# Performance work log

Hardware: AMD Instinct MI355X
Metric: run time of the kernel (lower is better)

The kernel has to match this reference:

```python
import jax, jax.numpy as jnp
import numpy as np

IN_F = 135; D = 512; K = 10; DCT_N = 34; IN_N = 120; OUT_N = 24
VL = K + OUT_N          # 34, window length
VN = IN_N - K - OUT_N + 1  # 87, number of windows
NSTAGE = 2
BN_SCALE = 1.0 / np.sqrt(1.0 + 1e-5)  # eval-mode BN with default running stats (mean 0, var 1)


def get_dct_matrix(N):
    dct_m = np.eye(N)
    for k in range(N):
        for i in range(N):
            w = np.sqrt(2.0 / N)
            if k == 0:
                w = np.sqrt(1.0 / N)
            dct_m[k, i] = w * np.cos(np.pi * (i + 0.5) * k / N)
    idct_m = np.linalg.inv(dct_m)
    return dct_m, idct_m

_DCT_NP, _IDCT_NP = get_dct_matrix(VL)
DCT = jnp.asarray(_DCT_NP[:DCT_N], dtype=jnp.float32)        # [34,34] (dct_n == vl)
IDCT = jnp.asarray(_IDCT_NP[:, :DCT_N], dtype=jnp.float32)   # [34,34]

WIN_IDX = np.arange(VL)[None, :] + np.arange(VN)[:, None]    # [87,34]
PAD_IDX = np.concatenate([np.arange(IN_N - K, IN_N), np.full(OUT_N, IN_N - 1)])  # last 10 frames + last frame repeated


def conv1d(x, w):
    return jax.lax.conv_general_dilated(x, w, (1,), 'VALID',
                                        dimension_numbers=('NCH', 'OIH', 'NCH'))


def gconv(x, att, w, b):
    # GraphConvolution: att @ (x @ w) + b ; x: [b,n,f_in]
    return jnp.einsum('nm,bmf->bnf', att, x @ w) + b


def bn_eval(y, g, b):
    bs, n, f = y.shape
    v = y.reshape(bs, n * f)
    v = g * (v * BN_SCALE) + b
    return v.reshape(bs, n, f)


def setup_inputs() -> dict:
    key = jax.random.key(0)
    ks = jax.random.split(key, 20)
    s = 0.05  # small init scale so tanh/att stay in sane range
    return {
        'poses':    jax.random.normal(ks[0], (256, 144, 135), jnp.float32),
        'qw1':      jax.random.normal(ks[1], (512, 135, 6)) * s,
        'qw2':      jax.random.normal(ks[2], (512, 512, 5)) * s,
        'kw1':      jax.random.normal(ks[3], (512, 135, 6)) * s,
        'kw2':      jax.random.normal(ks[4], (512, 512, 5)) * s,
        'gc1_att':  jax.random.normal(ks[5], (135, 135)) * s,
        'gc1_w':    jax.random.normal(ks[6], (68, 512)) * s,
        'gc1_b':    jax.random.normal(ks[7], (512,)) * s,
        'bn1_g':    jnp.ones((69120,), jnp.float32),
        'bn1_b':    jnp.zeros((69120,), jnp.float32),
        'gcb_att':  jax.random.normal(ks[8], (4, 135, 135)) * s,
        'gcb_w':    jax.random.normal(ks[9], (4, 512, 512)) * s,
        'gcb_b':    jax.random.normal(ks[10], (4, 512)) * s,
        'gcb_g':    jnp.ones((4, 69120), jnp.float32),
        'gcb_beta': jnp.zeros((4, 69120), jnp.float32),
        'gc7_att':  jax.random.normal(ks[11], (135, 135)) * s,
        'gc7_w':    jax.random.normal(ks[12], (512, 68)) * s,
        'gc7_b':    jax.random.normal(ks[13], (68,)) * s,
    }


def reference(poses, qw1, qw2, kw1, kw2,
              gc1_att, gc1_w, gc1_b, bn1_g, bn1_b,
              gcb_att, gcb_w, gcb_b, gcb_g, gcb_beta,
              gc7_att, gc7_w, gc7_b):
    src = poses[:, :IN_N]                      # [b,120,135]
    bs = src.shape[0]
    src_t = jnp.transpose(src, (0, 2, 1))      # [b,135,120]
    key_in = src_t[:, :, :IN_N - OUT_N] / 1000.0   # [b,135,96]
    qry_in = src_t[:, :, -K:] / 1000.0             # [b,135,10]

    key_f = jax.nn.relu(conv1d(jax.nn.relu(conv1d(key_in, kw1)), kw2))  # [b,512,87]
    qry_f = jax.nn.relu(conv1d(jax.nn.relu(conv1d(qry_in, qw1)), qw2))  # [b,512,1]

    # non-softmax attention: matmul + eps-normalize
    score = jnp.einsum('bdq,bdk->bqk', qry_f, key_f) + 1e-15   # [b,1,87]
    att = score / jnp.sum(score, axis=2, keepdims=True)

    # overlapping windows -> DCT of each window
    windows = src[:, WIN_IDX]                                   # [b,87,34,135]
    val = jnp.einsum('kt,bvtf->bvfk', DCT, windows).reshape(bs, VN, IN_F * DCT_N)
    dct_att = jnp.einsum('bqv,bvz->bqz', att, val)[:, 0].reshape(bs, IN_F, DCT_N)

    input_gcn = src[:, PAD_IDX]                                 # [b,34,135]
    dct_in = jnp.einsum('kt,btf->bfk', DCT, input_gcn)          # [b,135,34]
    x = jnp.concatenate([dct_in, dct_att], axis=-1)             # [b,135,68]

    # GCN (eval mode: dropout = identity, BN uses running stats)
    y = jnp.tanh(bn_eval(gconv(x, gc1_att, gc1_w, gc1_b), bn1_g, bn1_b))
    for i in range(NSTAGE):
        res = y
        h = jnp.tanh(bn_eval(gconv(y, gcb_att[2 * i], gcb_w[2 * i], gcb_b[2 * i]),
                             gcb_g[2 * i], gcb_beta[2 * i]))
        h = jnp.tanh(bn_eval(gconv(h, gcb_att[2 * i + 1], gcb_w[2 * i + 1], gcb_b[2 * i + 1]),
                             gcb_g[2 * i + 1], gcb_beta[2 * i + 1]))
        y = h + res
    y = gconv(y, gc7_att, gc7_w, gc7_b) + x                     # [b,135,68]

    out = jnp.einsum('tk,bfk->btf', IDCT, y[:, :, :DCT_N])      # [b,34,135]
    preds = out[:, -OUT_N:, :]                                  # [b,24,135]
    return preds
```

## Files before the change

kernel.cpp:

```cpp
#include <hip/hip_runtime.h>
#include <math.h>

#define POSE_ROWS 144
#define NF 135
#define DD 512
#define KQ 10
#define DCTN 34
#define INN 120
#define OUTN 24
#define VN 87
#define BATCH 256
#define RP 34816
#define NODEP 136
#define BSTRIDE 69632
#define BN_SCALE 0.9999950000374997f

typedef __attribute__((ext_vector_type(8))) short short8;
typedef __attribute__((ext_vector_type(4))) float floatx4;

static __device__ __forceinline__ ushort f2bf(float f) {
    unsigned u = __builtin_bit_cast(unsigned, f);
    u = (u + 0x7FFFu + ((u >> 16) & 1u)) >> 16;
    return (ushort)u;
}
static __device__ __forceinline__ float bf2f(ushort s) {
    return __builtin_bit_cast(float, (unsigned)s << 16);
}
static __device__ __forceinline__ float tanh_fast(float x) {
    float ax = __builtin_fabsf(x);
    float e = __builtin_amdgcn_exp2f(ax * -2.885390081777927f);
    float t = (1.f - e) * __builtin_amdgcn_rcpf(1.f + e);
    return __builtin_copysignf(t, x);
}

#define GLOAD_LDS(gp, lp) __builtin_amdgcn_global_load_lds( \
    (const __attribute__((address_space(1))) unsigned int*)(const void*)(gp), \
    (__attribute__((address_space(3))) unsigned int*)(void*)(lp), 16, 0, 0)

#define PB_POSES 19584
#define PB_K1B   22912
#define PB_K2B   33152
#define PB_WT1   33408
#define PB_WTB   37504
#define PB_WT7   37640
#define PB_A1    37742
#define PB_AB    38147
#define PB_A7    38249
#define PB_BN    39609
#define PB_Z     39610
#define PB_DCT   39615

__global__ __launch_bounds__(256) void prep_all(
    const float* __restrict__ poses, ushort* __restrict__ pb16,
    const float* __restrict__ kw1, const float* __restrict__ qw1,
    ushort* __restrict__ Wt1k, ushort* __restrict__ Wt1q,
    const float* __restrict__ kw2, const float* __restrict__ qw2,
    ushort* __restrict__ Wt2k, ushort* __restrict__ Wt2q,
    const float* __restrict__ gc1_w, ushort* __restrict__ WT1,
    const float* __restrict__ gcb_w, ushort* __restrict__ WTb,
    const float* __restrict__ gc7_w, ushort* __restrict__ WT7,
    const float* __restrict__ gc1_att, ushort* __restrict__ A16_1,
    const float* __restrict__ gcb_att, ushort* __restrict__ A16_B,
    const float* __restrict__ gc7_att, ushort* __restrict__ A16_7,
    const float* __restrict__ bn1_g, const float* __restrict__ bn1_b,
    const float* __restrict__ gcb_g, const float* __restrict__ gcb_beta,
    float* __restrict__ bnT, float* __restrict__ zpadf, float* __restrict__ dct)
{
    const int blk = blockIdx.x;
    const int tid = threadIdx.x;
    if (blk < PB_POSES) {
        int idx = blk * 256 + tid;
        int i = idx % NODEP;
        int row = (idx / NODEP) % POSE_ROWS;
        int b = idx / (NODEP * POSE_ROWS);
        float v = (i < NF) ? poses[((long long)b * POSE_ROWS + row) * NF + i] * 1e-3f : 0.f;
        pb16[idx] = f2bf(v);
    } else if (blk < PB_K1B) {
        int wi = blk - PB_POSES;
        const float* src = (wi < 1664) ? kw1 : qw1;
        ushort* dst = (wi < 1664) ? Wt1k : Wt1q;
        int idx = (wi % 1664) * 256 + tid;
        int n = idx / 832, k = idx % 832;
        int h = k / 136, i = k % 136;
        float v = (i < 135 && h < 6) ? src[((long long)n * 135 + i) * 6 + h] : 0.f;
        dst[idx] = f2bf(v);
    } else if (blk < PB_K2B) {
        int wi = blk - PB_K1B;
        const float* src = (wi < 5120) ? kw2 : qw2;
        ushort* dst = (wi < 5120) ? Wt2k : Wt2q;
        int idx = (wi % 5120) * 256 + tid;
        int n = idx / 2560, k = idx % 2560;
        int h = k / 512, i = k % 512;
        dst[idx] = f2bf(src[((long long)n * 512 + i) * 5 + h]);
    } else if (blk < PB_WT1) {
        int idx = (blk - PB_K2B) * 256 + tid;
        int n = idx / 128, k = idx % 128;
        WT1[idx] = f2bf((k < 68) ? gc1_w[(long long)k * 512 + n] : 0.f);
    } else if (blk < PB_WTB) {
        int g = (blk - PB_WT1) * 256 + tid;
        int L = g >> 18, idx = g & 262143;
        int n = idx / 512, k = idx % 512;
        WTb[g] = f2bf(gcb_w[(long long)L * 262144 + (long long)k * 512 + n]);
    } else if (blk < PB_WT7) {
        int idx = (blk - PB_WTB) * 256 + tid;
        int n = idx / 512, k = idx % 512;
        WT7[idx] = f2bf(gc7_w[(long long)k * 68 + n]);
    } else if (blk < PB_A1) {
        int idx = (blk - PB_WT7) * 256 + tid;
        if (idx < 135 * 192) {
            int r = idx / 192, c = idx % 192;
            A16_1[idx] = f2bf(c < 135 ? gc1_att[r * 135 + c] : 0.f);
        }
    } else if (blk < PB_AB) {
        int idx = (blk - PB_A1) * 256 + tid;
        int r = idx / 192, c = idx % 192;
        A16_B[idx] = f2bf(c < 135 ? gcb_att[r * 135 + c] : 0.f);
    } else if (blk < PB_A7) {
        int idx = (blk - PB_AB) * 256 + tid;
        if (idx < 135 * 192) {
            int r = idx / 192, c = idx % 192;
            A16_7[idx] = f2bf(c < 135 ? gc7_att[r * 135 + c] : 0.f);
        }
    } else if (blk < PB_BN) {
        int g = (blk - PB_A7) * 256 + tid;
        int p = g / 69632, idx = g % 69632;
        int node = idx % 136, m = idx / 136;
        const float* gs = (p == 0) ? bn1_g : (gcb_g + (p - 1) * 69120);
        const float* bs = (p == 0) ? bn1_b : (gcb_beta + (p - 1) * 69120);
        float* gt = bnT + (long long)p * 139264;
        float* bt = gt + 69632;
        gt[idx] = (node < 135) ? gs[node * 512 + m] : 0.f;
        bt[idx] = (node < 135) ? bs[node * 512 + m] : 0.f;
    } else if (blk < PB_Z) {
        if (tid < 128) zpadf[tid] = 0.f;
    } else {
        int idx = (blk - PB_Z) * 256 + tid;
        if (idx < DCTN * DCTN) {
            int k = idx / DCTN, i = idx % DCTN;
            double w = (k == 0) ? sqrt(1.0 / DCTN) : sqrt(2.0 / DCTN);
            dct[idx] = (float)(w * cos(3.14159265358979323846 * (i + 0.5) * k / (double)DCTN));
        }
    }
}

template<int BM, int BN>
__global__ __launch_bounds__(256) void gemm2(
    const ushort* __restrict__ A, const ushort* __restrict__ Bt,
    const ushort* __restrict__ zpad,
    int M, int N, int K,
    int mode, int CNT, int Pc,
    int rpbA, long long sAw, long long sAr, long long sAbz,
    long long sBr, long long sBbz,
    float* __restrict__ C, ushort* __restrict__ C16,
    long long sCbz, long long sCm, long long sCn,
    int do_relu, const float* __restrict__ bias, int bias_mode,
    const float* __restrict__ bnTg, const float* __restrict__ bnTb,
    int do_tanh, const ushort* __restrict__ resid16, const float* __restrict__ resid32,
    int bmaj)
{
    constexpr int SM = BM / 32, SN = BN / 32;
    constexpr int RA = BM / 32, RB = BN / 32;
    __shared__ ushort As[BM * 64];
    __shared__ ushort Bs[BN * 64];

    int mb, nb;
    if (mode == 0) { mb = blockIdx.y; nb = blockIdx.x; }
    else {
        int gx = blockIdx.x;
        int x = gx & 7, s = gx >> 3;
        if (mode == 1) { mb = s % CNT; nb = x * Pc + s / CNT; }
        else           { nb = s % CNT; mb = x * Pc + s / CNT; }
    }
    const int m0 = mb * BM, n0 = nb * BN;
    if (m0 >= M || n0 >= N) return;

    const int tid = threadIdx.x;
    const int lane = tid & 63, w = tid >> 6;
    const int bz = blockIdx.z;
    const int wm = (w >> 1) * (BM / 2), wn = (w & 1) * (BN / 2);
    const int chunk = (lane & 7) ^ ((lane >> 3) & 7);

    const ushort* pA[RA]; int stA[RA];
    #pragma unroll
    for (int j = 0; j < RA; j++) {
        int m = m0 + j * 32 + w * 8 + (lane >> 3);
        bool v = m < M;
        long long off = v ? ((long long)(m / rpbA) * sAw + (long long)(m % rpbA) * sAr
                            + (long long)bz * sAbz) : 0;
        pA[j] = v ? (A + off + chunk * 8) : (zpad + chunk * 8);
        stA[j] = v ? 64 : 0;
    }
    const ushort* pB[RB]; int stB[RB];
    #pragma unroll
    for (int j = 0; j < RB; j++) {
        int n = n0 + j * 32 + w * 8 + (lane >> 3);
        bool v = n < N;
        long long off = v ? ((long long)n * sBr + (long long)bz * sBbz) : 0;
        pB[j] = v ? (Bt + off + chunk * 8) : (zpad + chunk * 8);
        stB[j] = v ? 64 : 0;
    }

    floatx4 acc[SM][SN];
    #pragma unroll
    for (int i = 0; i < SM; i++)
        #pragma unroll
        for (int j = 0; j < SN; j++)
            acc[i][j] = (floatx4){0.f, 0.f, 0.f, 0.f};

    for (int k0 = 0; k0 < K; k0 += 64) {
        #pragma unroll
        for (int j = 0; j < RA; j++)
            GLOAD_LDS(pA[j], &As[(j * 32 + w * 8) * 64]);
        #pragma unroll
        for (int j = 0; j < RB; j++)
            GLOAD_LDS(pB[j], &Bs[(j * 32 + w * 8) * 64]);
        __syncthreads();

        #pragma unroll
        for (int kk = 0; kk < 2; kk++) {
            short8 af[SM], bf[SN];
            #pragma unroll
            for (int sm = 0; sm < SM; sm++) {
                int lr = wm + sm * 16 + (lane & 15);
                int slot = ((lane >> 4) + kk * 4) ^ (lr & 7);
                af[sm] = *(const short8*)&As[lr * 64 + slot * 8];
            }
            #pragma unroll
            for (int sn = 0; sn < SN; sn++) {
                int lr = wn + sn * 16 + (lane & 15);
                int slot = ((lane >> 4) + kk * 4) ^ (lr & 7);
                bf[sn] = *(const short8*)&Bs[lr * 64 + slot * 8];
            }
            #pragma unroll
            for (int sm = 0; sm < SM; sm++)
                #pragma unroll
                for (int sn = 0; sn < SN; sn++)
                    acc[sm][sn] = __builtin_amdgcn_mfma_f32_16x16x32_bf16(af[sm], bf[sn], acc[sm][sn], 0, 0, 0);
        }
        __syncthreads();

        #pragma unroll
        for (int j = 0; j < RA; j++) pA[j] += stA[j];
        #pragma unroll
        for (int j = 0; j < RB; j++) pB[j] += stB[j];
    }

    const int lc = lane & 15;
    const int lr4 = (lane >> 4) << 2;
    #pragma unroll
    for (int sm = 0; sm < SM; sm++) {
        #pragma unroll
        for (int sn = 0; sn < SN; sn++) {
            int n = n0 + wn + sn * 16 + lc;
            if (n >= N) continue;
            int node = n % 136;
            int mbv = m0 + wm + sm * 16 + lr4;
            float vv[4];
            #pragma unroll
            for (int r = 0; r < 4; r++) {
                int m = mbv + r;
                float v = acc[sm][sn][r];
                if (do_relu) v = fmaxf(v, 0.f);
                if (bias) v += (bias_mode == 1) ? bias[m < M ? m : 0] : bias[n];
                if (bnTg) {
                    long long gi = (long long)(m < M ? m : 0) * 136 + node;
                    v = bnTg[gi] * (v * BN_SCALE) + bnTb[gi];
                }
                if (do_tanh) v = tanh_fast(v);
                long long addr = bmaj
                    ? (long long)(n / 136) * BSTRIDE + (long long)m * 136 + node
                    : (long long)bz * sCbz + (long long)m * sCm + (long long)n * sCn;
                if (m < M) {
                    if (resid16) v += bf2f(resid16[addr]);
                    else if (resid32) v += resid32[addr];
                    if (C) C[addr] = v;
                    if (C16 && sCm != 1) C16[addr] = f2bf(v);
                }
                vv[r] = v;
            }
            if (C16 && sCm == 1 && mbv + 3 < M) {
                ushort4 pk;
                pk.x = f2bf(vv[0]); pk.y = f2bf(vv[1]); pk.z = f2bf(vv[2]); pk.w = f2bf(vv[3]);
                *(ushort4*)&C16[(long long)bz * sCbz + mbv + (long long)n * sCn] = pk;
            }
        }
    }
}

__global__ __launch_bounds__(512) void fused_layer(
    const ushort* __restrict__ Yin,
    const ushort* __restrict__ Att,
    const ushort* __restrict__ Wt,
    const ushort* __restrict__ zpad,
    const float* __restrict__ bias,
    const float* __restrict__ bnTg, const float* __restrict__ bnTb,
    const ushort* __restrict__ resid16,
    ushort* __restrict__ Yout)
{
    extern __shared__ ushort zs[];
    const int b = blockIdx.x;
    const int tid = threadIdx.x;
    const int lane = tid & 63, w = tid >> 6;
    const int ln = lane & 15;
    const int lk8 = (lane >> 4) * 8;
    const int lr4 = (lane >> 4) << 2;
    const long long ybase = (long long)b * BSTRIDE;
    const int cp = w * 64;

    {
        const ushort* pb[9];
        #pragma unroll
        for (int nt = 0; nt < 9; nt++) {
            int n = nt * 16 + ln;
            pb[nt] = (n < 135) ? (Att + (long long)n * 192 + lk8) : (zpad + lk8);
        }
        const ushort* pa[4];
        #pragma unroll
        for (int sm = 0; sm < 4; sm++) {
            int c = cp + sm * 16 + ln;
            pa[sm] = Yin + ybase + (long long)c * 136 + lk8;
        }
        floatx4 acc[4][9];
        #pragma unroll
        for (int i = 0; i < 4; i++)
            #pragma unroll
            for (int j = 0; j < 9; j++)
                acc[i][j] = (floatx4){0.f, 0.f, 0.f, 0.f};

        #pragma unroll
        for (int ks = 0; ks < 5; ks++) {
            const int ko = ks * 32;
            short8 af[4];
            #pragma unroll
            for (int sm = 0; sm < 4; sm++)
                af[sm] = *(const short8*)(pa[sm] + ko);
            #pragma unroll
            for (int nt = 0; nt < 9; nt++) {
                short8 bfv = *(const short8*)(pb[nt] + ko);
                #pragma unroll
                for (int sm = 0; sm < 4; sm++)
                    acc[sm][nt] = __builtin_amdgcn_mfma_f32_16x16x32_bf16(af[sm], bfv, acc[sm][nt], 0, 0, 0);
            }
        }
        #pragma unroll
        for (int sm = 0; sm < 4; sm++) {
            #pragma unroll
            for (int nt = 0; nt < 9; nt++) {
                int n = nt * 16 + ln;
                if (n >= 136) continue;
                int c = cp + sm * 16 + lr4;
                ushort4 pk;
                pk.x = f2bf(acc[sm][nt][0]);
                pk.y = f2bf(acc[sm][nt][1]);
                pk.z = f2bf(acc[sm][nt][2]);
                pk.w = f2bf(acc[sm][nt][3]);
                int chs = (c >> 3) ^ (n & 7);
                *(ushort4*)&zs[n * 512 + chs * 8 + (c & 7)] = pk;
            }
        }
    }
    __syncthreads();

    {
        const ushort* pw[4];
        #pragma unroll
        for (int sm = 0; sm < 4; sm++)
            pw[sm] = Wt + (long long)(cp + sm * 16 + ln) * 512 + lk8;
        int zrow[9], zx[9];
        #pragma unroll
        for (int nt = 0; nt < 9; nt++) {
            int n = nt * 16 + ln;
            int nn = (n < 136) ? n : 0;
            zrow[nt] = nn * 512;
            zx[nt] = nn & 7;
        }
        floatx4 acc[4][9];
        #pragma unroll
        for (int i = 0; i < 4; i++)
            #pragma unroll
            for (int j = 0; j < 9; j++)
                acc[i][j] = (floatx4){0.f, 0.f, 0.f, 0.f};

        #pragma unroll
        for (int ks = 0; ks < 16; ks++) {
            const int ko = ks * 32;
            const int kchunk = ks * 4 + (lane >> 4);
            short8 af[4];
            #pragma unroll
            for (int sm = 0; sm < 4; sm++)
                af[sm] = *(const short8*)(pw[sm] + ko);
            #pragma unroll
            for (int nt = 0; nt < 9; nt++) {
                short8 bfv = *(const short8*)&zs[zrow[nt] + (kchunk ^ zx[nt]) * 8];
                #pragma unroll
                for (int sm = 0; sm < 4; sm++)
                    acc[sm][nt] = __builtin_amdgcn_mfma_f32_16x16x32_bf16(af[sm], bfv, acc[sm][nt], 0, 0, 0);
            }
        }
        #pragma unroll
        for (int sm = 0; sm < 4; sm++) {
            #pragma unroll
            for (int nt = 0; nt < 9; nt++) {
                int n = nt * 16 + ln;
                if (n >= 136) continue;
                int c2 = cp + sm * 16 + lr4;
                #pragma unroll
                for (int r = 0; r < 4; r++) {
                    int m = c2 + r;
                    float v = acc[sm][nt][r];
                    v += bias[m];
                    long long gi = (long long)m * 136 + n;
                    v = bnTg[gi] * (v * BN_SCALE) + bnTb[gi];
                    v = tanh_fast(v);
                    long long addr = ybase + (long long)m * 136 + n;
                    if (resid16) v += bf2f(resid16[addr]);
                    Yout[addr] = f2bf(v);
                }
            }
        }
    }
}

__global__ __launch_bounds__(256) void att_k(const float* __restrict__ kf, const float* __restrict__ qf,
                                             float* __restrict__ att) {
    int b = blockIdx.x;
    int tid = threadIdx.x;
    int lane = tid & 63, w = tid >> 6;
    __shared__ float s[96];
    __shared__ float ssum;
    const float* qb = qf + b * DD + lane * 8;
    float4 q0 = *(const float4*)qb;
    float4 q1 = *(const float4*)(qb + 4);
    const float* kb = kf + (long long)b * VN * DD;
    for (int v = w; v < VN; v += 4) {
        const float* kr = kb + v * DD + lane * 8;
        float4 k0 = *(const float4*)kr;
        float4 k1 = *(const float4*)(kr + 4);
        float p = q0.x * k0.x + q0.y * k0.y + q0.z * k0.z + q0.w * k0.w
                + q1.x * k1.x + q1.y * k1.y + q1.z * k1.z + q1.w * k1.w;
        #pragma unroll
        for (int off = 32; off; off >>= 1) p += __shfl_xor(p, off);
        if (lane == 0) s[v] = p + 1e-15f;
    }
    __syncthreads();
    if (tid < 64) {
        float p2 = (tid < VN ? s[tid] : 0.f) + ((tid + 64) < VN ? s[tid + 64] : 0.f);
        #pragma unroll
        for (int off = 32; off; off >>= 1) p2 += __shfl_xor(p2, off);
        if (tid == 0) ssum = p2;
    }
    __syncthreads();
    float inv = 1.f / ssum;
    for (int v = tid; v < VN; v += 256) att[b * VN + v] = s[v] * inv;
}

__global__ void weighted_k(const float* __restrict__ poses, const float* __restrict__ att,
                           float* __restrict__ w34) {
    int t = blockIdx.x;
    int b = blockIdx.y;
    int f = threadIdx.x;
    if (f >= NF) return;
    const float* pb = poses + (long long)b * POSE_ROWS * NF + t * NF + f;
    const float* ab = att + b * VN;
    float acc = 0.f;
    for (int v = 0; v < VN; v++) acc += ab[v] * pb[v * NF];
    w34[(long long)b * DCTN * NF + t * NF + f] = acc;
}

__global__ void build_x(const float* __restrict__ poses, const float* __restrict__ w34,
                        const float* __restrict__ dctm, float* __restrict__ x32,
                        ushort* __restrict__ xT16) {
    int idx = blockIdx.x * 256 + threadIdx.x;
    if (idx >= BATCH * NF * 68) return;
    int kk = idx % 68;
    int f = (idx / 68) % NF;
    int b = idx / (68 * NF);
    float acc = 0.f;
    if (kk < DCTN) {
        const float* pb = poses + (long long)b * POSE_ROWS * NF;
        #pragma unroll
        for (int t = 0; t < DCTN; t++) {
            int row = (t < KQ) ? (INN - KQ + t) : (INN - 1);
            acc += dctm[kk * DCTN + t] * pb[row * NF + f];
        }
    } else {
        int k2 = kk - DCTN;
        const float* wb = w34 + (long long)b * DCTN * NF + f;
        #pragma unroll
        for (int t = 0; t < DCTN; t++) acc += dctm[k2 * DCTN + t] * wb[t * NF];
    }
    long long R = (long long)b * NODEP + f;
    x32[R * 68 + kk] = acc;
    xT16[(long long)kk * RP + R] = f2bf(acc);
}

__global__ void idct_out(const float* __restrict__ h32, const float* __restrict__ dctm,
                         float* __restrict__ out) {
    int idx = blockIdx.x * 256 + threadIdx.x;
    if (idx >= BATCH * OUTN * NF) return;
    int f = idx % NF;
    int t = (idx / NF) % OUTN;
    int b = idx / (NF * OUTN);
    const float* yr = h32 + ((long long)b * NODEP + f) * 68;
    float acc = 0.f;
    #pragma unroll
    for (int k = 0; k < DCTN; k++) acc += dctm[k * DCTN + (KQ + t)] * yr[k];
    out[idx] = acc;
}

extern "C" void kernel_launch(void* const* d_in, const int* in_sizes, int n_in,
                              void* d_out, int out_size, void* d_ws, size_t ws_size,
                              hipStream_t stream) {
    const float* poses   = (const float*)d_in[0];
    const float* qw1     = (const float*)d_in[1];
    const float* qw2     = (const float*)d_in[2];
    const float* kw1     = (const float*)d_in[3];
    const float* kw2     = (const float*)d_in[4];
    const float* gc1_att = (const float*)d_in[5];
    const float* gc1_w   = (const float*)d_in[6];
    const float* gc1_b   = (const float*)d_in[7];
    const float* bn1_g   = (const float*)d_in[8];
    const float* bn1_b   = (const float*)d_in[9];
    const float* gcb_att = (const float*)d_in[10];
    const float* gcb_w   = (const float*)d_in[11];
    const float* gcb_b   = (const float*)d_in[12];
    const float* gcb_g   = (const float*)d_in[13];
    const float* gcb_beta= (const float*)d_in[14];
    const float* gc7_att = (const float*)d_in[15];
    const float* gc7_w   = (const float*)d_in[16];
    const float* gc7_b   = (const float*)d_in[17];
    float* out = (float*)d_out;
    float* w = (float*)d_ws;

    float* dct   = w;
    float* att   = w + 1280;
    float* w34   = w + 23808;
    float* x32   = w + 1198848;
    float* h32   = w + 3566336;
    float* qf    = w + 5933824;
    ushort* su   = (ushort*)(w + 6064896);
    ushort* WT1    = su;
    ushort* WTb    = su + 65536;
    ushort* WT7    = su + 1114112;
    ushort* A16_1  = su + 1148928;
    ushort* A16_B  = su + 1174848;
    ushort* A16_7  = su + 1278528;
    float* bnT   = w + 6717120;
    float* kf    = w + 7413440;
    ushort* R2   = (ushort*)(w + 18816704);
    ushort* yT16  = R2;
    ushort* r1k16 = R2;
    ushort* r1q16 = R2 + 11927552;
    ushort* R3   = (ushort*)(w + 27729600);
    ushort* hT16  = R3;
    ushort* pb16  = R3;
    ushort* Wt1k  = R3 + 5013504;
    ushort* Wt1q  = R3 + 5439488;
    ushort* Wt2k  = R3 + 5865472;
    ushort* Wt2q  = R3 + 7176192;
    ushort* R4   = (ushort*)(w + 36642496);
    ushort* zN16  = R4;
    ushort* xT16  = R4;
    ushort* z116  = R4 + 2367488;
    float* zpadf = w + 45555392;
    const ushort* zpad = (const ushort*)zpadf;

    const int INF_RPB = 1 << 30;

    static int lds_set = 0;
    if (!lds_set) {
        hipFuncSetAttribute((const void*)fused_layer,
                            hipFuncAttributeMaxDynamicSharedMemorySize, 139264);
        lds_set = 1;
    }

    prep_all<<<PB_DCT, 256, 0, stream>>>(
        poses, pb16, kw1, qw1, Wt1k, Wt1q, kw2, qw2, Wt2k, Wt2q,
        gc1_w, WT1, gcb_w, WTb, gc7_w, WT7,
        gc1_att, A16_1, gcb_att, A16_B, gc7_att, A16_7,
        bn1_g, bn1_b, gcb_g, gcb_beta, bnT, zpadf, dct);

    gemm2<128,64><<<dim3(1472, 1, 1), 256, 0, stream>>>(pb16, Wt1k, zpad, 23296, 512, 832,
        2, 8, 23, 91, 19584LL, 136LL, 0LL, 832LL, 0LL,
        (float*)nullptr, r1k16, 0LL, 512LL, 1LL, 1, nullptr, 0, nullptr, nullptr, 0, nullptr, nullptr, 0);
    gemm2<128,128><<<dim3(4, 10, 1), 256, 0, stream>>>(pb16 + 110*136, Wt1q, zpad, 1280, 512, 832,
        0, 0, 0, 5, 19584LL, 136LL, 0LL, 832LL, 0LL,
        (float*)nullptr, r1q16, 0LL, 512LL, 1LL, 1, nullptr, 0, nullptr, nullptr, 0, nullptr, nullptr, 0);
    gemm2<128,64><<<dim3(1408, 1, 1), 256, 0, stream>>>(r1k16, Wt2k, zpad, 22272, 512, 2560,
        2, 8, 22, 87, 46592LL, 512LL, 0LL, 2560LL, 0LL,
        kf, (ushort*)nullptr, 0LL, 512LL, 1LL, 1, nullptr, 0, nullptr, nullptr, 0, nullptr, nullptr, 0);
    gemm2<64,64><<<dim3(8, 4, 1), 256, 0, stream>>>(r1q16, Wt2q, zpad, 256, 512, 2560,
        0, 0, 0, INF_RPB, 0LL, 2560LL, 0LL, 2560LL, 0LL,
        qf, (ushort*)nullptr, 0LL, 512LL, 1LL, 1, nullptr, 0, nullptr, nullptr, 0, nullptr, nullptr, 0);

    att_k<<<BATCH, 256, 0, stream>>>(kf, qf, att);
    weighted_k<<<dim3(DCTN, BATCH), 192, 0, stream>>>(poses, att, w34);
    build_x<<<(BATCH * NF * 68 + 255) / 256, 256, 0, stream>>>(poses, w34, dct, x32, xT16);

    gemm2<64,64><<<dim3(3, 2, BATCH), 256, 0, stream>>>(xT16, A16_1, zpad, 68, 135, 192,
        0, 0, 0, INF_RPB, 0LL, (long long)RP, 136LL, 192LL, 0LL,
        (float*)nullptr, z116, 10880LL, 1LL, 80LL, 0, nullptr, 0, nullptr, nullptr, 0, nullptr, nullptr, 0);
    gemm2<128,64><<<dim3(2176, 1, 1), 256, 0, stream>>>(WT1, z116, zpad, 512, RP, 128,
        1, 4, 68, INF_RPB, 0LL, 128LL, 0LL, 80LL, 0LL,
        (float*)nullptr, yT16, 0LL, (long long)RP, 1LL, 0, gc1_b, 1, bnT, bnT + 69632, 1, nullptr, nullptr, 1);

    for (int L = 0; L < 4; L++) {
        const ushort* min = (L & 1) ? hT16 : yT16;
        ushort* mout = (L & 1) ? yT16 : hT16;
        fused_layer<<<dim3(BATCH, 1, 1), 512, 139264, stream>>>(
            min, A16_B + L * 25920, WTb + L * 262144, zpad,
            gcb_b + L * 512, bnT + (1 + L) * 139264, bnT + (1 + L) * 139264 + 69632,
            (L & 1) ? yT16 : (const ushort*)nullptr, mout);
    }

    gemm2<64,64><<<dim3(3, 8, BATCH), 256, 0, stream>>>(yT16, A16_7, zpad, 512, 135, 192,
        0, 0, 0, INF_RPB, 0LL, 136LL, (long long)BSTRIDE, 192LL, 0LL,
        (float*)nullptr, zN16, 69632LL, 1LL, 512LL, 0, nullptr, 0, nullptr, nullptr, 0, nullptr, nullptr, 0);
    gemm2<64,64><<<dim3(1088, 1, 1), 256, 0, stream>>>(zN16, WT7, zpad, RP, 68, 512,
        2, 2, 68, INF_RPB, 0LL, 512LL, 0LL, 512LL, 0LL,
        h32, (ushort*)nullptr, 0LL, 68LL, 1LL, 0, gc7_b, 2, nullptr, nullptr, 0, nullptr, x32, 0);

    idct_out<<<(BATCH * OUTN * NF + 255) / 256, 256, 0, stream>>>(h32, dct, out);
}
```

Measured before the change: 896.4 us.

## Fold bias and BN scale into interleaved gain/shift, double-buffer fused layer A loads

```diff
diff --git a/kernel.cpp b/kernel.cpp
--- a/kernel.cpp
+++ b/kernel.cpp
@@ -31,6 +31,9 @@
     float e = __builtin_amdgcn_exp2f(ax * -2.885390081777927f);
     float t = (1.f - e) * __builtin_amdgcn_rcpf(1.f + e);
     return __builtin_copysignf(t, x);
+}
+static __device__ __forceinline__ floatx4 mf(short8 a, short8 b, floatx4 c) {
+    return __builtin_amdgcn_mfma_f32_16x16x32_bf16(a, b, c, 0, 0, 0);
 }
 
 #define GLOAD_LDS(gp, lp) __builtin_amdgcn_global_load_lds( \
@@ -64,6 +67,7 @@
     const float* __restrict__ gc7_att, ushort* __restrict__ A16_7,
     const float* __restrict__ bn1_g, const float* __restrict__ bn1_b,
     const float* __restrict__ gcb_g, const float* __restrict__ gcb_beta,
+    const float* __restrict__ gc1_bias, const float* __restrict__ gcb_bias,
     float* __restrict__ bnT, float* __restrict__ zpadf, float* __restrict__ dct)
 {
     const int blk = blockIdx.x;
@@ -127,10 +131,13 @@
         int node = idx % 136, m = idx / 136;
         const float* gs = (p == 0) ? bn1_g : (gcb_g + (p - 1) * 69120);
         const float* bs = (p == 0) ? bn1_b : (gcb_beta + (p - 1) * 69120);
+        const float* bp = (p == 0) ? gc1_bias : (gcb_bias + (p - 1) * 512);
         float* gt = bnT + (long long)p * 139264;
-        float* bt = gt + 69632;
-        gt[idx] = (node < 135) ? gs[node * 512 + m] : 0.f;
-        bt[idx] = (node < 135) ? bs[node * 512 + m] : 0.f;
+        float gg = (node < 135) ? gs[node * 512 + m] : 0.f;
+        float bb = (node < 135) ? bs[node * 512 + m] : 0.f;
+        float gx = gg * BN_SCALE;
+        gt[idx * 2]     = gx;
+        gt[idx * 2 + 1] = gx * bp[m] + bb;
     } else if (blk < PB_Z) {
         if (tid < 128) zpadf[tid] = 0.f;
     } else {
@@ -235,7 +242,7 @@
             for (int sm = 0; sm < SM; sm++)
                 #pragma unroll
                 for (int sn = 0; sn < SN; sn++)
-                    acc[sm][sn] = __builtin_amdgcn_mfma_f32_16x16x32_bf16(af[sm], bf[sn], acc[sm][sn], 0, 0, 0);
+                    acc[sm][sn] = mf(af[sm], bf[sn], acc[sm][sn]);
         }
         __syncthreads();
 
@@ -264,7 +271,8 @@
                 if (bias) v += (bias_mode == 1) ? bias[m < M ? m : 0] : bias[n];
                 if (bnTg) {
                     long long gi = (long long)(m < M ? m : 0) * 136 + node;
-                    v = bnTg[gi] * (v * BN_SCALE) + bnTb[gi];
+                    float2 gbv = ((const float2*)bnTg)[gi];
+                    v = gbv.x * v + gbv.y;
                 }
                 if (do_tanh) v = tanh_fast(v);
                 long long addr = bmaj
@@ -292,8 +300,7 @@
     const ushort* __restrict__ Att,
     const ushort* __restrict__ Wt,
     const ushort* __restrict__ zpad,
-    const float* __restrict__ bias,
-    const float* __restrict__ bnTg, const float* __restrict__ bnTb,
+    const float2* __restrict__ bnGB,
     const ushort* __restrict__ resid16,
     ushort* __restrict__ Yout)
 {
@@ -327,21 +334,36 @@
             for (int j = 0; j < 9; j++)
                 acc[i][j] = (floatx4){0.f, 0.f, 0.f, 0.f};
 
-        #pragma unroll
-        for (int ks = 0; ks < 5; ks++) {
+        auto p1load = [&](int ks, short8 (&AF)[4]) {
             const int ko = ks * 32;
-            short8 af[4];
             #pragma unroll
             for (int sm = 0; sm < 4; sm++)
-                af[sm] = *(const short8*)(pa[sm] + ko);
-            #pragma unroll
-            for (int nt = 0; nt < 9; nt++) {
-                short8 bfv = *(const short8*)(pb[nt] + ko);
+                AF[sm] = *(const short8*)(pa[sm] + ko);
+        };
+        auto p1comp = [&](int ks, short8 (&AF)[4]) {
+            const int ko = ks * 32;
+            short8 bf[9];
+            #pragma unroll
+            for (int nt = 0; nt < 9; nt++)
+                bf[nt] = *(const short8*)(pb[nt] + ko);
+            #pragma unroll
+            for (int nt = 0; nt < 9; nt++)
                 #pragma unroll
                 for (int sm = 0; sm < 4; sm++)
-                    acc[sm][nt] = __builtin_amdgcn_mfma_f32_16x16x32_bf16(af[sm], bfv, acc[sm][nt], 0, 0, 0);
-            }
-        }
+                    acc[sm][nt] = mf(AF[sm], bf[nt], acc[sm][nt]);
+        };
+        short8 afA[4], afB[4];
+        p1load(0, afA);
+        p1load(1, afB);
+        p1comp(0, afA);
+        p1load(2, afA);
+        p1comp(1, afB);
+        p1load(3, afB);
+        p1comp(2, afA);
+        p1load(4, afA);
+        p1comp(3, afB);
+        p1comp(4, afA);
+
         #pragma unroll
         for (int sm = 0; sm < 4; sm++) {
             #pragma unroll
@@ -381,42 +403,64 @@
             for (int j = 0; j < 9; j++)
                 acc[i][j] = (floatx4){0.f, 0.f, 0.f, 0.f};
 
-        #pragma unroll
-        for (int ks = 0; ks < 16; ks++) {
+        auto p2load = [&](int ks, short8 (&AF)[4]) {
             const int ko = ks * 32;
+            #pragma unroll
+            for (int sm = 0; sm < 4; sm++)
+                AF[sm] = *(const short8*)(pw[sm] + ko);
+        };
+        auto p2comp = [&](int ks, short8 (&AF)[4]) {
             const int kchunk = ks * 4 + (lane >> 4);
-            short8 af[4];
-            #pragma unroll
-            for (int sm = 0; sm < 4; sm++)
-                af[sm] = *(const short8*)(pw[sm] + ko);
-            #pragma unroll
-            for (int nt = 0; nt < 9; nt++) {
-                short8 bfv = *(const short8*)&zs[zrow[nt] + (kchunk ^ zx[nt]) * 8];
+            short8 bf[9];
+            #pragma unroll
+            for (int nt = 0; nt < 9; nt++)
+                bf[nt] = *(const short8*)&zs[zrow[nt] + (kchunk ^ zx[nt]) * 8];
+            #pragma unroll
+            for (int nt = 0; nt < 9; nt++)
                 #pragma unroll
                 for (int sm = 0; sm < 4; sm++)
-                    acc[sm][nt] = __builtin_amdgcn_mfma_f32_16x16x32_bf16(af[sm], bfv, acc[sm][nt], 0, 0, 0);
-            }
-        }
-        #pragma unroll
-        for (int sm = 0; sm < 4; sm++) {
-            #pragma unroll
-            for (int nt = 0; nt < 9; nt++) {
-                int n = nt * 16 + ln;
-                if (n >= 136) continue;
-                int c2 = cp + sm * 16 + lr4;
+                    acc[sm][nt] = mf(AF[sm], bf[nt], acc[sm][nt]);
+        };
+        short8 afA[4], afB[4];
+        p2load(0, afA);
+        p2load(1, afB);
+        #pragma unroll
+        for (int kp = 0; kp < 7; kp++) {
+            p2comp(2 * kp, afA);
+            p2load(2 * kp + 2, afA);
+            p2comp(2 * kp + 1, afB);
+            p2load(2 * kp + 3, afB);
+        }
+        p2comp(14, afA);
+        p2comp(15, afB);
+
+        #pragma unroll
+        for (int nt = 0; nt < 9; nt++) {
+            int n = nt * 16 + ln;
+            int nn = (n < 136) ? n : 0;
+            float2 gb[16];
+            ushort rr[16];
+            #pragma unroll
+            for (int sm = 0; sm < 4; sm++)
                 #pragma unroll
                 for (int r = 0; r < 4; r++) {
-                    int m = c2 + r;
+                    int m = cp + sm * 16 + lr4 + r;
+                    gb[sm * 4 + r] = bnGB[(long long)m * 136 + nn];
+                    rr[sm * 4 + r] = resid16 ? resid16[ybase + (long long)m * 136 + nn]
+                                             : (ushort)0;
+                }
+            if (n >= 136) continue;
+            #pragma unroll
+            for (int sm = 0; sm < 4; sm++)
+                #pragma unroll
+                for (int r = 0; r < 4; r++) {
+                    int m = cp + sm * 16 + lr4 + r;
                     float v = acc[sm][nt][r];
-                    v += bias[m];
-                    long long gi = (long long)m * 136 + n;
-                    v = bnTg[gi] * (v * BN_SCALE) + bnTb[gi];
+                    v = gb[sm * 4 + r].x * v + gb[sm * 4 + r].y;
                     v = tanh_fast(v);
-                    long long addr = ybase + (long long)m * 136 + n;
-                    if (resid16) v += bf2f(resid16[addr]);
-                    Yout[addr] = f2bf(v);
+                    if (resid16) v += bf2f(rr[sm * 4 + r]);
+                    Yout[ybase + (long long)m * 136 + n] = f2bf(v);
                 }
-            }
         }
     }
 }
@@ -578,7 +622,7 @@
         poses, pb16, kw1, qw1, Wt1k, Wt1q, kw2, qw2, Wt2k, Wt2q,
         gc1_w, WT1, gcb_w, WTb, gc7_w, WT7,
         gc1_att, A16_1, gcb_att, A16_B, gc7_att, A16_7,
-        bn1_g, bn1_b, gcb_g, gcb_beta, bnT, zpadf, dct);
+        bn1_g, bn1_b, gcb_g, gcb_beta, gc1_b, gcb_b, bnT, zpadf, dct);
 
     gemm2<128,64><<<dim3(1472, 1, 1), 256, 0, stream>>>(pb16, Wt1k, zpad, 23296, 512, 832,
         2, 8, 23, 91, 19584LL, 136LL, 0LL, 832LL, 0LL,
@@ -602,14 +646,14 @@
         (float*)nullptr, z116, 10880LL, 1LL, 80LL, 0, nullptr, 0, nullptr, nullptr, 0, nullptr, nullptr, 0);
     gemm2<128,64><<<dim3(2176, 1, 1), 256, 0, stream>>>(WT1, z116, zpad, 512, RP, 128,
         1, 4, 68, INF_RPB, 0LL, 128LL, 0LL, 80LL, 0LL,
-        (float*)nullptr, yT16, 0LL, (long long)RP, 1LL, 0, gc1_b, 1, bnT, bnT + 69632, 1, nullptr, nullptr, 1);
+        (float*)nullptr, yT16, 0LL, (long long)RP, 1LL, 0, nullptr, 0, bnT, nullptr, 1, nullptr, nullptr, 1);
 
     for (int L = 0; L < 4; L++) {
         const ushort* min = (L & 1) ? hT16 : yT16;
         ushort* mout = (L & 1) ? yT16 : hT16;
         fused_layer<<<dim3(BATCH, 1, 1), 512, 139264, stream>>>(
             min, A16_B + L * 25920, WTb + L * 262144, zpad,
-            gcb_b + L * 512, bnT + (1 + L) * 139264, bnT + (1 + L) * 139264 + 69632,
+            (const float2*)(bnT + (1 + L) * 139264),
             (L & 1) ? yT16 : (const ushort*)nullptr, mout);
     }
 
```

Measured after the change: 823.6 us. 8.1% less time.
